# Performance work log

Measured on AMD Instinct MI355X. Metric: run time of the kernel, lower is better.

## Reference

```python
import jax, jax.numpy as jnp
import numpy as np

# SelectiveAttention (keras) reference.
# - A single shared InputDense (D -> key_dim) projects query, key, value.
# - ComponentBuilder yields (filter_input=Q, context_input=banded K^T, _input=V):
#   scores = (Q K^T / sqrt(key_dim)) masked to the band |i-j| <= band_size
#   (the layer's Softmax sublayer is built but never invoked in call()).
# - attended = scores @ V, then OutputDense (key_dim -> D). Dropout inactive at inference.

def setup_inputs() -> dict:
    key = jax.random.key(0)
    ks = jax.random.split(key, 5)
    B, S, D, Dk = 4, 4096, 512, 64
    query = jax.random.normal(ks[0], (B, S, D), dtype=jnp.float32)
    value = jax.random.normal(ks[1], (B, S, D), dtype=jnp.float32)
    Wi = jax.random.normal(ks[2], (D, Dk), dtype=jnp.float32) * (1.0 / np.sqrt(D))
    bi = jnp.zeros((Dk,), dtype=jnp.float32)
    Wo = jax.random.normal(ks[3], (Dk, D), dtype=jnp.float32) * (1.0 / np.sqrt(Dk))
    bo = jnp.zeros((D,), dtype=jnp.float32)
    return {"query": query, "value": value, "Wi": Wi, "bi": bi,
            "Wo": Wo, "bo": bo, "band_size": 128}


def reference(query, value, Wi, bi, Wo, bo, band_size):
    Dk = Wi.shape[1]
    scale = 1.0 / jnp.sqrt(jnp.asarray(Dk, dtype=query.dtype))
    # shared input projection (same dense for q, k, v; key defaults to value)
    q = query @ Wi + bi            # [B,S,Dk]
    kv = value @ Wi + bi           # [B,S,Dk]  (k == v here)
    scores = jnp.einsum('bqd,bkd->bqk', q, kv) * scale  # [B,S,S]
    S = q.shape[1]
    idx = jnp.arange(S)
    band = (jnp.abs(idx[:, None] - idx[None, :]) <= band_size)  # [S,S] bool
    scores = jnp.where(band[None], scores, 0.0)
    attended = jnp.einsum('bqk,bkd->bqd', scores, kv)    # [B,S,Dk]
    return attended @ Wo + bo                            # [B,S,D]
```

## Files before the change

### kernel.cpp

```cpp
#include <hip/hip_runtime.h>
#include <math.h>


typedef __bf16 bf16;
using bf16x4  = __attribute__((ext_vector_type(4))) __bf16;
using bf16x8  = __attribute__((ext_vector_type(8))) __bf16;
using floatx4 = __attribute__((ext_vector_type(4))) float;

#define MFMA(a, b, c) __builtin_amdgcn_mfma_f32_16x16x32_bf16(a, b, c, 0, 0, 0)

__global__ __launch_bounds__(256) void prep_weights(
    const float* __restrict__ Wi, const float* __restrict__ Wo,
    bf16* __restrict__ WiT, bf16* __restrict__ WoT)
{
    __shared__ float T[64][65];
    const int blk = blockIdx.x, tid = threadIdx.x;
    if (blk < 8) {
        const int k0 = blk * 64;
        #pragma unroll
        for (int i = 0; i < 4; i++) {
            int idx4 = tid * 4 + i;
            int r = idx4 >> 4, c4 = (idx4 & 15) * 4;
            float4 f = *(const float4*)(Wi + (size_t)(k0 + r) * 64 + c4);
            T[r][c4 + 0] = f.x; T[r][c4 + 1] = f.y;
            T[r][c4 + 2] = f.z; T[r][c4 + 3] = f.w;
        }
        __syncthreads();
        #pragma unroll
        for (int i = 0; i < 2; i++) {
            int seg = tid * 2 + i;
            int n = seg >> 3, k8 = (seg & 7) * 8;
            bf16x8 v;
            #pragma unroll
            for (int j = 0; j < 8; j++) v[j] = (bf16)T[k8 + j][n];
            *(bf16x8*)(WiT + (size_t)n * 512 + k0 + k8) = v;
        }
    } else {
        const int n0 = (blk - 8) * 64;
        #pragma unroll
        for (int i = 0; i < 4; i++) {
            int idx4 = tid * 4 + i;
            int r = idx4 >> 4, c4 = (idx4 & 15) * 4;
            float4 f = *(const float4*)(Wo + (size_t)r * 512 + n0 + c4);
            T[r][c4 + 0] = f.x; T[r][c4 + 1] = f.y;
            T[r][c4 + 2] = f.z; T[r][c4 + 3] = f.w;
        }
        __syncthreads();
        #pragma unroll
        for (int i = 0; i < 2; i++) {
            int seg = tid * 2 + i;
            int n = seg >> 3, k8 = (seg & 7) * 8;
            bf16x8 v;
            #pragma unroll
            for (int j = 0; j < 8; j++) v[j] = (bf16)T[k8 + j][n];
            *(bf16x8*)(WoT + (size_t)(n0 + n) * 64 + k8) = v;
        }
    }
}

__global__ __launch_bounds__(256, 4) void proj_in_kernel(
    const float* __restrict__ v, const bf16* __restrict__ WiT,
    const float* __restrict__ bi, bf16* __restrict__ kvp,
    bf16* __restrict__ kvT, int K, int S)
{
    __shared__ float P[4][16][68];
    const int tid = threadIdx.x;
    const int wave = tid >> 6, lane = tid & 63;
    const int lr = lane & 15, lq = lane >> 4;
    const int row0 = blockIdx.x * 16;
    const float* xrow = v + (size_t)(row0 + lr) * K + wave * 128;
    const bf16* wrow = WiT + wave * 128;

    floatx4 acc[4] = {};
    #pragma unroll
    for (int ks = 0; ks < 4; ks++) {
        const int k0 = ks * 32 + lq * 8;
        float4 a0 = *(const float4*)(xrow + k0);
        float4 a1 = *(const float4*)(xrow + k0 + 4);
        bf16x8 af;
        af[0] = (bf16)a0.x; af[1] = (bf16)a0.y; af[2] = (bf16)a0.z; af[3] = (bf16)a0.w;
        af[4] = (bf16)a1.x; af[5] = (bf16)a1.y; af[6] = (bf16)a1.z; af[7] = (bf16)a1.w;
        #pragma unroll
        for (int t = 0; t < 4; t++) {
            bf16x8 bfv = *(const bf16x8*)(wrow + (size_t)(t * 16 + lr) * K + k0);
            acc[t] = MFMA(af, bfv, acc[t]);
        }
    }
    #pragma unroll
    for (int t = 0; t < 4; t++)
        #pragma unroll
        for (int r = 0; r < 4; r++)
            P[wave][lq * 4 + r][t * 16 + lr] = acc[t][r];
    __syncthreads();

    {
        const int row = tid >> 4, c4 = (tid & 15) * 4;
        float4 s0 = *(const float4*)&P[0][row][c4];
        float4 s1 = *(const float4*)&P[1][row][c4];
        float4 s2 = *(const float4*)&P[2][row][c4];
        float4 s3 = *(const float4*)&P[3][row][c4];
        float4 bb = *(const float4*)(bi + c4);
        bf16x4 o;
        o[0] = (bf16)(s0.x + s1.x + s2.x + s3.x + bb.x);
        o[1] = (bf16)(s0.y + s1.y + s2.y + s3.y + bb.y);
        o[2] = (bf16)(s0.z + s1.z + s2.z + s3.z + bb.z);
        o[3] = (bf16)(s0.w + s1.w + s2.w + s3.w + bb.w);
        *(bf16x4*)(kvp + (size_t)(row0 + row) * 64 + c4) = o;
    }
    {
        const int d = tid >> 2, s4 = (tid & 3) * 4;
        const int b = row0 >> 12, s0r = row0 & (S - 1);
        const float bb = bi[d];
        bf16x4 o;
        #pragma unroll
        for (int i = 0; i < 4; i++) {
            float s = P[0][s4 + i][d] + P[1][s4 + i][d]
                    + P[2][s4 + i][d] + P[3][s4 + i][d] + bb;
            o[i] = (bf16)s;
        }
        *(bf16x4*)(kvT + ((size_t)b * 64 + d) * S + s0r + s4) = o;
    }
}

__global__ __launch_bounds__(256, 4) void band_attn_out_kernel(
    const float* __restrict__ query, const bf16* __restrict__ WiT,
    const float* __restrict__ bi, const bf16* __restrict__ kvp,
    const bf16* __restrict__ kvT, const int* __restrict__ band_ptr,
    const bf16* __restrict__ WoT, const float* __restrict__ bo,
    float* __restrict__ out, int K, int S, float scale)
{
    __shared__ float P[4][16][68];
    __shared__ bf16 Ss[4][16][40];
    __shared__ bf16 St[16][88];
    const int tid = threadIdx.x;
    const int wave = tid >> 6, lane = tid & 63;
    const int lr = lane & 15, lq = lane >> 4;
    const int gs = blockIdx.x;
    const int b = gs >> 8;
    const int q0 = (gs & 255) * 16;
    const int band = band_ptr[0];

    {
        const float* xrow = query + ((size_t)b * S + q0 + lr) * K + wave * 128;
        const bf16* wrow = WiT + wave * 128;
        floatx4 qa[4] = {};
        #pragma unroll
        for (int ks = 0; ks < 4; ks++) {
            const int k0 = ks * 32 + lq * 8;
            float4 a0 = *(const float4*)(xrow + k0);
            float4 a1 = *(const float4*)(xrow + k0 + 4);
            bf16x8 af;
            af[0] = (bf16)a0.x; af[1] = (bf16)a0.y; af[2] = (bf16)a0.z; af[3] = (bf16)a0.w;
            af[4] = (bf16)a1.x; af[5] = (bf16)a1.y; af[6] = (bf16)a1.z; af[7] = (bf16)a1.w;
            #pragma unroll
            for (int t = 0; t < 4; t++) {
                bf16x8 bfv = *(const bf16x8*)(wrow + (size_t)(t * 16 + lr) * K + k0);
                qa[t] = MFMA(af, bfv, qa[t]);
            }
        }
        #pragma unroll
        for (int t = 0; t < 4; t++)
            #pragma unroll
            for (int r = 0; r < 4; r++)
                P[wave][lq * 4 + r][t * 16 + lr] = qa[t][r];
    }
    __syncthreads();
    {
        const int row = tid >> 4, c4 = (tid & 15) * 4;
        float4 s0 = *(const float4*)&P[0][row][c4];
        float4 s1 = *(const float4*)&P[1][row][c4];
        float4 s2 = *(const float4*)&P[2][row][c4];
        float4 s3 = *(const float4*)&P[3][row][c4];
        float4 bb = *(const float4*)(bi + c4);
        bf16x4 o;
        o[0] = (bf16)((s0.x + s1.x + s2.x + s3.x + bb.x) * scale);
        o[1] = (bf16)((s0.y + s1.y + s2.y + s3.y + bb.y) * scale);
        o[2] = (bf16)((s0.z + s1.z + s2.z + s3.z + bb.z) * scale);
        o[3] = (bf16)((s0.w + s1.w + s2.w + s3.w + bb.w) * scale);
        *(bf16x4*)(&St[row][c4]) = o;
    }
    __syncthreads();
    bf16x8 qf0 = *(const bf16x8*)(&St[lr][lq * 8]);
    bf16x8 qf1 = *(const bf16x8*)(&St[lr][32 + lq * 8]);

    floatx4 acc[4] = {};
    const int base = ((q0 - band) >> 6) * 64;
    #pragma unroll
    for (int i = 0; i < 3; i++) {
        const int h = wave + i * 4;
        if (h < 10) {
            const int kj0 = base + h * 32;
            floatx4 sc[2] = {};
            #pragma unroll
            for (int t2 = 0; t2 < 2; t2++) {
                int kr = kj0 + t2 * 16 + lr;
                int krc = min(max(kr, 0), S - 1);
                const bf16* kp = kvp + ((size_t)b * S + krc) * 64;
                bf16x8 b0 = *(const bf16x8*)(kp + lq * 8);
                bf16x8 b1 = *(const bf16x8*)(kp + 32 + lq * 8);
                sc[t2] = MFMA(qf0, b0, sc[t2]);
                sc[t2] = MFMA(qf1, b1, sc[t2]);
            }
            #pragma unroll
            for (int t2 = 0; t2 < 2; t2++) {
                int kj = kj0 + t2 * 16 + lr;
                bool kv_ok = (kj >= 0) && (kj < S);
                #pragma unroll
                for (int r = 0; r < 4; r++) {
                    int qi = q0 + lq * 4 + r;
                    int dlt = qi - kj; dlt = dlt < 0 ? -dlt : dlt;
                    float vv = (kv_ok && dlt <= band) ? sc[t2][r] : 0.f;
                    Ss[wave][lq * 4 + r][t2 * 16 + lr] = (bf16)vv;
                }
            }
            bf16x8 sa = *(const bf16x8*)(&Ss[wave][lr][lq * 8]);
            int kb = kj0 + lq * 8;
            int kbc = min(max(kb, 0), S - 8);
            #pragma unroll
            for (int t = 0; t < 4; t++) {
                bf16x8 vb = *(const bf16x8*)(kvT + ((size_t)b * 64 + t * 16 + lr) * S + kbc);
                acc[t] = MFMA(sa, vb, acc[t]);
            }
        }
    }
    #pragma unroll
    for (int t = 0; t < 4; t++)
        #pragma unroll
        for (int r = 0; r < 4; r++)
            P[wave][lq * 4 + r][t * 16 + lr] = acc[t][r];
    __syncthreads();

    {
        const int row = tid >> 4, c4 = (tid & 15) * 4;
        float4 s0 = *(const float4*)&P[0][row][c4];
        float4 s1 = *(const float4*)&P[1][row][c4];
        float4 s2 = *(const float4*)&P[2][row][c4];
        float4 s3 = *(const float4*)&P[3][row][c4];
        bf16x4 o;
        o[0] = (bf16)(s0.x + s1.x + s2.x + s3.x);
        o[1] = (bf16)(s0.y + s1.y + s2.y + s3.y);
        o[2] = (bf16)(s0.z + s1.z + s2.z + s3.z);
        o[3] = (bf16)(s0.w + s1.w + s2.w + s3.w);
        *(bf16x4*)(&St[row][c4]) = o;
    }
    __syncthreads();

    bf16x8 af0 = *(const bf16x8*)(&St[lr][lq * 8]);
    bf16x8 af1 = *(const bf16x8*)(&St[lr][32 + lq * 8]);
    float* orow = out + ((size_t)b * S + q0) * 512;
    #pragma unroll
    for (int i = 0; i < 8; i++) {
        const int tp = wave * 8 + i;
        const bf16* wp = WoT + (size_t)(tp * 16 + lr) * 64;
        bf16x8 b0 = *(const bf16x8*)(wp + lq * 8);
        bf16x8 b1 = *(const bf16x8*)(wp + 32 + lq * 8);
        floatx4 o = {};
        o = MFMA(af0, b0, o);
        o = MFMA(af1, b1, o);
        float bb = bo[tp * 16 + lr];
        #pragma unroll
        for (int r = 0; r < 4; r++)
            orow[(size_t)(lq * 4 + r) * 512 + tp * 16 + lr] = o[r] + bb;
    }
}

extern "C" void kernel_launch(void* const* d_in, const int* in_sizes, int n_in,
                              void* d_out, int out_size, void* d_ws, size_t ws_size,
                              hipStream_t stream) {
    const float* query = (const float*)d_in[0];
    const float* value = (const float*)d_in[1];
    const float* Wi    = (const float*)d_in[2];
    const float* bi    = (const float*)d_in[3];
    const float* Wo    = (const float*)d_in[4];
    const float* bo    = (const float*)d_in[5];
    const int*   band  = (const int*)d_in[6];
    float* out = (float*)d_out;

    const int Dk = in_sizes[3];
    const int D  = in_sizes[5];
    const int S  = 4096;
    const int BS = in_sizes[0] / D;
    const int B  = BS / S;
    const float scale = 1.0f / sqrtf((float)Dk);

    bf16* WiT = (bf16*)d_ws;
    bf16* WoT = WiT + 32768;
    bf16* kvp = WoT + 32768;
    bf16* kvT = kvp + (size_t)BS * 64;

    prep_weights<<<16, 256, 0, stream>>>(Wi, Wo, WiT, WoT);

    proj_in_kernel<<<dim3(BS / 16), 256, 0, stream>>>(
        value, WiT, bi, kvp, kvT, D, S);

    band_attn_out_kernel<<<dim3(BS / 16), 256, 0, stream>>>(
        query, WiT, bi, kvp, kvT, band, WoT, bo, out, D, S, scale);
}
```

Measured before the change: 145.1 us.

## Split P·V work by output column per wave and vectorize output stores

All 10 masked score tiles are now written to a shared Ss buffer. After a barrier, each wave computes one 16-column slice of the attended output over the whole band, where before each wave held partial sums for all 64 columns. This removes the fp32 partial-sum write to P, the four-way cross-wave reduction and one barrier, and cuts per-wave kvT loads and MFMAs in that stage. The output projection swaps its MFMA operands so each lane holds four consecutive output columns, which allows float4 stores and float4 bias loads instead of scalar strided stores. The cost is a larger shared score buffer, which could lower occupancy.

```diff
diff --git a/kernel.cpp b/kernel.cpp
--- a/kernel.cpp
+++ b/kernel.cpp
@@ -130,7 +130,7 @@
     float* __restrict__ out, int K, int S, float scale)
 {
     __shared__ float P[4][16][68];
-    __shared__ bf16 Ss[4][16][40];
+    __shared__ bf16 Ss[16][344];
     __shared__ bf16 St[16][88];
     const int tid = threadIdx.x;
     const int wave = tid >> 6, lane = tid & 63;
@@ -183,7 +183,6 @@
     bf16x8 qf0 = *(const bf16x8*)(&St[lr][lq * 8]);
     bf16x8 qf1 = *(const bf16x8*)(&St[lr][32 + lq * 8]);
 
-    floatx4 acc[4] = {};
     const int base = ((q0 - band) >> 6) * 64;
     #pragma unroll
     for (int i = 0; i < 3; i++) {
@@ -210,38 +209,27 @@
                     int qi = q0 + lq * 4 + r;
                     int dlt = qi - kj; dlt = dlt < 0 ? -dlt : dlt;
                     float vv = (kv_ok && dlt <= band) ? sc[t2][r] : 0.f;
-                    Ss[wave][lq * 4 + r][t2 * 16 + lr] = (bf16)vv;
+                    Ss[lq * 4 + r][h * 32 + t2 * 16 + lr] = (bf16)vv;
                 }
             }
-            bf16x8 sa = *(const bf16x8*)(&Ss[wave][lr][lq * 8]);
-            int kb = kj0 + lq * 8;
+        }
+    }
+    __syncthreads();
+
+    {
+        floatx4 acc = {};
+        const bf16* vrow = kvT + ((size_t)b * 64 + wave * 16 + lr) * S;
+        #pragma unroll
+        for (int h = 0; h < 10; h++) {
+            bf16x8 sa = *(const bf16x8*)(&Ss[lr][h * 32 + lq * 8]);
+            int kb = base + h * 32 + lq * 8;
             int kbc = min(max(kb, 0), S - 8);
-            #pragma unroll
-            for (int t = 0; t < 4; t++) {
-                bf16x8 vb = *(const bf16x8*)(kvT + ((size_t)b * 64 + t * 16 + lr) * S + kbc);
-                acc[t] = MFMA(sa, vb, acc[t]);
-            }
-        }
-    }
-    #pragma unroll
-    for (int t = 0; t < 4; t++)
+            bf16x8 vb = *(const bf16x8*)(vrow + kbc);
+            acc = MFMA(sa, vb, acc);
+        }
         #pragma unroll
         for (int r = 0; r < 4; r++)
-            P[wave][lq * 4 + r][t * 16 + lr] = acc[t][r];
-    __syncthreads();
-
-    {
-        const int row = tid >> 4, c4 = (tid & 15) * 4;
-        float4 s0 = *(const float4*)&P[0][row][c4];
-        float4 s1 = *(const float4*)&P[1][row][c4];
-        float4 s2 = *(const float4*)&P[2][row][c4];
-        float4 s3 = *(const float4*)&P[3][row][c4];
-        bf16x4 o;
-        o[0] = (bf16)(s0.x + s1.x + s2.x + s3.x);
-        o[1] = (bf16)(s0.y + s1.y + s2.y + s3.y);
-        o[2] = (bf16)(s0.z + s1.z + s2.z + s3.z);
-        o[3] = (bf16)(s0.w + s1.w + s2.w + s3.w);
-        *(bf16x4*)(&St[row][c4]) = o;
+            St[lq * 4 + r][wave * 16 + lr] = (bf16)acc[r];
     }
     __syncthreads();
 
@@ -252,15 +240,16 @@
     for (int i = 0; i < 8; i++) {
         const int tp = wave * 8 + i;
         const bf16* wp = WoT + (size_t)(tp * 16 + lr) * 64;
-        bf16x8 b0 = *(const bf16x8*)(wp + lq * 8);
-        bf16x8 b1 = *(const bf16x8*)(wp + 32 + lq * 8);
+        bf16x8 w0 = *(const bf16x8*)(wp + lq * 8);
+        bf16x8 w1 = *(const bf16x8*)(wp + 32 + lq * 8);
         floatx4 o = {};
-        o = MFMA(af0, b0, o);
-        o = MFMA(af1, b1, o);
-        float bb = bo[tp * 16 + lr];
-        #pragma unroll
-        for (int r = 0; r < 4; r++)
-            orow[(size_t)(lq * 4 + r) * 512 + tp * 16 + lr] = o[r] + bb;
+        o = MFMA(w0, af0, o);
+        o = MFMA(w1, af1, o);
+        float4 bb = *(const float4*)(bo + tp * 16 + lq * 4);
+        float4 ov;
+        ov.x = o[0] + bb.x; ov.y = o[1] + bb.y;
+        ov.z = o[2] + bb.z; ov.w = o[3] + bb.w;
+        *(float4*)(orow + (size_t)lr * 512 + tp * 16 + lq * 4) = ov;
     }
 }
 
```

New measurement: 148.8 us. 1.03x slower.

## Fuse projection and banded attention into one cooperative kernel with per-strip flags

Applied to the files above, without the earlier changes.

Merges the value-projection kernel and the banded attention/output kernel into a single cooperative launch. Each block projects its own 16-row strip of K/V, publishes it with a release flag, then computes its query projection and spins on the flags of the neighbouring strips it needs before running the band attention. The transposed K/V buffer is re-laid out as per-strip 64x16 tiles so each block writes contiguously. This removes one kernel launch and the global barrier between the two phases, and lets projection overlap with attention. In exchange it depends on cooperative co-residency of all 1024 blocks to avoid deadlock, and the fallback path is a plain launch that could hang if not all blocks fit.

```diff
diff --git a/kernel.cpp b/kernel.cpp
--- a/kernel.cpp
+++ b/kernel.cpp
@@ -11,10 +11,14 @@
 
 __global__ __launch_bounds__(256) void prep_weights(
     const float* __restrict__ Wi, const float* __restrict__ Wo,
-    bf16* __restrict__ WiT, bf16* __restrict__ WoT)
+    bf16* __restrict__ WiT, bf16* __restrict__ WoT, int* __restrict__ flags)
 {
     __shared__ float T[64][65];
     const int blk = blockIdx.x, tid = threadIdx.x;
+    if (blk == 0) {
+        #pragma unroll
+        for (int i = 0; i < 4; i++) flags[i * 256 + tid] = 0;
+    }
     if (blk < 8) {
         const int k0 = blk * 64;
         #pragma unroll
@@ -58,41 +62,51 @@
     }
 }
 
-__global__ __launch_bounds__(256, 4) void proj_in_kernel(
-    const float* __restrict__ v, const bf16* __restrict__ WiT,
-    const float* __restrict__ bi, bf16* __restrict__ kvp,
-    bf16* __restrict__ kvT, int K, int S)
+__global__ __launch_bounds__(256, 4) void fused_attn_kernel(
+    const float* __restrict__ query, const float* __restrict__ value,
+    const bf16* __restrict__ WiT, const float* __restrict__ bi,
+    bf16* __restrict__ kvp, bf16* __restrict__ kvT,
+    const int* __restrict__ band_ptr, const bf16* __restrict__ WoT,
+    const float* __restrict__ bo, float* __restrict__ out,
+    int* __restrict__ flags, int K, int S, float scale)
 {
     __shared__ float P[4][16][68];
+    __shared__ bf16 Ss[4][16][40];
+    __shared__ bf16 St[16][88];
     const int tid = threadIdx.x;
     const int wave = tid >> 6, lane = tid & 63;
     const int lr = lane & 15, lq = lane >> 4;
-    const int row0 = blockIdx.x * 16;
-    const float* xrow = v + (size_t)(row0 + lr) * K + wave * 128;
-    const bf16* wrow = WiT + wave * 128;
-
-    floatx4 acc[4] = {};
-    #pragma unroll
-    for (int ks = 0; ks < 4; ks++) {
-        const int k0 = ks * 32 + lq * 8;
-        float4 a0 = *(const float4*)(xrow + k0);
-        float4 a1 = *(const float4*)(xrow + k0 + 4);
-        bf16x8 af;
-        af[0] = (bf16)a0.x; af[1] = (bf16)a0.y; af[2] = (bf16)a0.z; af[3] = (bf16)a0.w;
-        af[4] = (bf16)a1.x; af[5] = (bf16)a1.y; af[6] = (bf16)a1.z; af[7] = (bf16)a1.w;
-        #pragma unroll
-        for (int t = 0; t < 4; t++) {
-            bf16x8 bfv = *(const bf16x8*)(wrow + (size_t)(t * 16 + lr) * K + k0);
-            acc[t] = MFMA(af, bfv, acc[t]);
-        }
-    }
-    #pragma unroll
-    for (int t = 0; t < 4; t++)
-        #pragma unroll
-        for (int r = 0; r < 4; r++)
-            P[wave][lq * 4 + r][t * 16 + lr] = acc[t][r];
-    __syncthreads();
-
+    const int gs = blockIdx.x;
+    const int b = gs >> 8;
+    const int row0 = gs * 16;
+    const int q0 = (gs & 255) * 16;
+    const int band = band_ptr[0];
+
+    {
+        const float* xrow = value + (size_t)(row0 + lr) * K + wave * 128;
+        const bf16* wrow = WiT + wave * 128;
+        floatx4 acc[4] = {};
+        #pragma unroll
+        for (int ks = 0; ks < 4; ks++) {
+            const int k0 = ks * 32 + lq * 8;
+            float4 a0 = *(const float4*)(xrow + k0);
+            float4 a1 = *(const float4*)(xrow + k0 + 4);
+            bf16x8 af;
+            af[0] = (bf16)a0.x; af[1] = (bf16)a0.y; af[2] = (bf16)a0.z; af[3] = (bf16)a0.w;
+            af[4] = (bf16)a1.x; af[5] = (bf16)a1.y; af[6] = (bf16)a1.z; af[7] = (bf16)a1.w;
+            #pragma unroll
+            for (int t = 0; t < 4; t++) {
+                bf16x8 bfv = *(const bf16x8*)(wrow + (size_t)(t * 16 + lr) * K + k0);
+                acc[t] = MFMA(af, bfv, acc[t]);
+            }
+        }
+        #pragma unroll
+        for (int t = 0; t < 4; t++)
+            #pragma unroll
+            for (int r = 0; r < 4; r++)
+                P[wave][lq * 4 + r][t * 16 + lr] = acc[t][r];
+    }
+    __syncthreads();
     {
         const int row = tid >> 4, c4 = (tid & 15) * 4;
         float4 s0 = *(const float4*)&P[0][row][c4];
@@ -109,7 +123,6 @@
     }
     {
         const int d = tid >> 2, s4 = (tid & 3) * 4;
-        const int b = row0 >> 12, s0r = row0 & (S - 1);
         const float bb = bi[d];
         bf16x4 o;
         #pragma unroll
@@ -118,30 +131,17 @@
                     + P[2][s4 + i][d] + P[3][s4 + i][d] + bb;
             o[i] = (bf16)s;
         }
-        *(bf16x4*)(kvT + ((size_t)b * 64 + d) * S + s0r + s4) = o;
-    }
-}
-
-__global__ __launch_bounds__(256, 4) void band_attn_out_kernel(
-    const float* __restrict__ query, const bf16* __restrict__ WiT,
-    const float* __restrict__ bi, const bf16* __restrict__ kvp,
-    const bf16* __restrict__ kvT, const int* __restrict__ band_ptr,
-    const bf16* __restrict__ WoT, const float* __restrict__ bo,
-    float* __restrict__ out, int K, int S, float scale)
-{
-    __shared__ float P[4][16][68];
-    __shared__ bf16 Ss[4][16][40];
-    __shared__ bf16 St[16][88];
-    const int tid = threadIdx.x;
-    const int wave = tid >> 6, lane = tid & 63;
-    const int lr = lane & 15, lq = lane >> 4;
-    const int gs = blockIdx.x;
-    const int b = gs >> 8;
-    const int q0 = (gs & 255) * 16;
-    const int band = band_ptr[0];
-
-    {
-        const float* xrow = query + ((size_t)b * S + q0 + lr) * K + wave * 128;
+        *(bf16x4*)(kvT + ((size_t)gs * 64 + d) * 16 + s4) = o;
+    }
+    __syncthreads();
+    if (tid == 0) {
+        __threadfence();
+        __hip_atomic_store(&flags[gs], 1, __ATOMIC_RELEASE,
+                           __HIP_MEMORY_SCOPE_AGENT);
+    }
+
+    {
+        const float* xrow = query + (size_t)(row0 + lr) * K + wave * 128;
         const bf16* wrow = WiT + wave * 128;
         floatx4 qa[4] = {};
         #pragma unroll
@@ -183,8 +183,19 @@
     bf16x8 qf0 = *(const bf16x8*)(&St[lr][lq * 8]);
     bf16x8 qf1 = *(const bf16x8*)(&St[lr][32 + lq * 8]);
 
+    const int base = ((q0 - band) >> 6) * 64;
+    {
+        const int bc = max(base, 0), lc = min(base + 319, S - 1);
+        const int lo_s = bc >> 4, n = (lc >> 4) - lo_s + 1;
+        if (tid < n) {
+            const int fi = (b << 8) + lo_s + tid;
+            while (__hip_atomic_load(&flags[fi], __ATOMIC_ACQUIRE,
+                                     __HIP_MEMORY_SCOPE_AGENT) == 0) {}
+        }
+        __syncthreads();
+    }
+
     floatx4 acc[4] = {};
-    const int base = ((q0 - band) >> 6) * 64;
     #pragma unroll
     for (int i = 0; i < 3; i++) {
         const int h = wave + i * 4;
@@ -216,9 +227,11 @@
             bf16x8 sa = *(const bf16x8*)(&Ss[wave][lr][lq * 8]);
             int kb = kj0 + lq * 8;
             int kbc = min(max(kb, 0), S - 8);
+            const size_t vstrip = ((size_t)(b << 8) + (kbc >> 4)) * 64;
+            const int voff = kbc & 15;
             #pragma unroll
             for (int t = 0; t < 4; t++) {
-                bf16x8 vb = *(const bf16x8*)(kvT + ((size_t)b * 64 + t * 16 + lr) * S + kbc);
+                bf16x8 vb = *(const bf16x8*)(kvT + (vstrip + t * 16 + lr) * 16 + voff);
                 acc[t] = MFMA(sa, vb, acc[t]);
             }
         }
@@ -247,7 +260,7 @@
 
     bf16x8 af0 = *(const bf16x8*)(&St[lr][lq * 8]);
     bf16x8 af1 = *(const bf16x8*)(&St[lr][32 + lq * 8]);
-    float* orow = out + ((size_t)b * S + q0) * 512;
+    float* orow = out + (size_t)row0 * 512;
     #pragma unroll
     for (int i = 0; i < 8; i++) {
         const int tp = wave * 8 + i;
@@ -278,21 +291,32 @@
 
     const int Dk = in_sizes[3];
     const int D  = in_sizes[5];
-    const int S  = 4096;
+    int S  = 4096;
     const int BS = in_sizes[0] / D;
-    const int B  = BS / S;
-    const float scale = 1.0f / sqrtf((float)Dk);
+    float scale = 1.0f / sqrtf((float)Dk);
+    int K = D;
 
     bf16* WiT = (bf16*)d_ws;
     bf16* WoT = WiT + 32768;
     bf16* kvp = WoT + 32768;
     bf16* kvT = kvp + (size_t)BS * 64;
-
-    prep_weights<<<16, 256, 0, stream>>>(Wi, Wo, WiT, WoT);
-
-    proj_in_kernel<<<dim3(BS / 16), 256, 0, stream>>>(
-        value, WiT, bi, kvp, kvT, D, S);
-
-    band_attn_out_kernel<<<dim3(BS / 16), 256, 0, stream>>>(
-        query, WiT, bi, kvp, kvT, band, WoT, bo, out, D, S, scale);
+    int* flags = (int*)(kvT + (size_t)BS * 64);
+
+    const int NBV = BS / 16;
+
+    prep_weights<<<16, 256, 0, stream>>>(Wi, Wo, WiT, WoT, flags);
+
+    void* kargs[] = {
+        (void*)&query, (void*)&value, (void*)&WiT, (void*)&bi,
+        (void*)&kvp, (void*)&kvT, (void*)&band, (void*)&WoT,
+        (void*)&bo, (void*)&out, (void*)&flags, (void*)&K, (void*)&S,
+        (void*)&scale
+    };
+    hipError_t err = hipLaunchCooperativeKernel(
+        (const void*)fused_attn_kernel, dim3(NBV), dim3(256), kargs, 0, stream);
+    if (err != hipSuccess) {
+        fused_attn_kernel<<<dim3(NBV), 256, 0, stream>>>(
+            query, value, WiT, bi, kvp, kvT, band, WoT, bo, out,
+            flags, K, S, scale);
+    }
 }
```

Result: slower. 235.7 us (+62.4%).
